# Performance work log

Measured on AMD Instinct MI355X. Metric: run time of the kernel, lower is better.

The kernel has to match this reference:

```python
import jax, jax.numpy as jnp
import numpy as np

B, NNODE, FIN, FOUT = 64, 512, 64, 64

def setup_inputs() -> dict:
    key = jax.random.key(0)
    ks = jax.random.split(key, 8)
    stdW = 1.0 / np.sqrt(FIN)
    stdA = 1.0 / np.sqrt(FOUT)
    return {
        "X": jax.random.normal(ks[0], (B, NNODE, FIN), dtype=jnp.float32),
        "A": jax.random.uniform(ks[1], (B, NNODE, NNODE), dtype=jnp.float32),
        "N": jax.random.randint(ks[2], (B,), 1, NNODE + 1, dtype=jnp.int64),
        "W": jax.random.uniform(ks[3], (FIN, FOUT), jnp.float32, -stdW, stdW),
        "a": jax.random.uniform(ks[4], (FOUT, FOUT), jnp.float32, -stdA, stdA),
        "bias_W": jax.random.uniform(ks[5], (FOUT,), jnp.float32, -stdW, stdW),
        "bias_a": jax.random.uniform(ks[6], (NNODE,), jnp.float32, -1.0 / np.sqrt(NNODE), 1.0 / np.sqrt(NNODE)),
    }

def reference(X, A, N, W, a, bias_W, bias_a):
    # A_ = A + identity on the top-left n_atoms block (only diagonal entries)
    idx = jnp.arange(A.shape[1])
    diag_mask = (idx[None, :] < N[:, None]).astype(A.dtype)  # [B, n]
    A_ = A + jnp.einsum('bn,nm->bnm', diag_mask, jnp.eye(A.shape[1], dtype=A.dtype))
    # XW: [B, n, F_out]
    XW = jnp.einsum('bnc,cd->bnd', X, W)
    # buf[a,j,k] = sum_i a[i,j] * XW^T[a,j,k]  (einsum 'ij,ajk->ajk')
    col_sum = a.sum(axis=0)  # [F_out]
    XWT = jnp.swapaxes(XW, 1, 2)  # [B, F_out, n]
    buf = col_sum[None, :, None] * XWT
    Z = jnp.einsum('bif,bfk->bik', XW, buf) + bias_a  # [B, n, n] + [n] broadcast on last dim
    att = jnp.tanh(jnp.einsum('bij,bjk->bik', A_, Z))
    H = jnp.einsum('bij,bjd->bid', att, XW) + bias_W
    return H
```

## Files before the change

kernel.cpp:

```cpp
#include <hip/hip_runtime.h>

#define BB 64
#define NN 512
#define FD 64

typedef short bf16x8 __attribute__((ext_vector_type(8)));
typedef float f32x4 __attribute__((ext_vector_type(4)));

__device__ __forceinline__ unsigned short f2bf(float f){
    unsigned u = __builtin_bit_cast(unsigned, f);
    u += 0x7fffu + ((u >> 16) & 1u);
    return (unsigned short)(u >> 16);
}
__device__ __forceinline__ float bf2f(unsigned short h){
    unsigned u = ((unsigned)h) << 16;
    return __builtin_bit_cast(float, u);
}
__device__ __forceinline__ float fast_tanh(float x){
    float e = __expf(2.0f * x);
    return 1.0f - 2.0f * __builtin_amdgcn_rcpf(e + 1.0f);
}

__global__ __launch_bounds__(256) void k_xw(const float* __restrict__ X,
                                            const float* __restrict__ W,
                                            unsigned short* __restrict__ XWh,
                                            unsigned short* __restrict__ XWt){
    __shared__ unsigned short Xl[64][72];
    __shared__ unsigned short Wtl[64][72];
    __shared__ unsigned short Cl[64][72];
    __shared__ unsigned short ClT[64][72];
    int t = threadIdx.x;
    int row0 = blockIdx.x * 64;
    int r = t >> 2, c0 = (t & 3) * 16;
    {
        const float4* wsrc = (const float4*)&W[r*64 + c0];
        #pragma unroll
        for (int q = 0; q < 4; q++){
            float4 v = wsrc[q];
            Wtl[c0 + q*4 + 0][r] = f2bf(v.x);
            Wtl[c0 + q*4 + 1][r] = f2bf(v.y);
            Wtl[c0 + q*4 + 2][r] = f2bf(v.z);
            Wtl[c0 + q*4 + 3][r] = f2bf(v.w);
        }
        const float4* src = (const float4*)&X[(row0 + r)*FD + c0];
        #pragma unroll
        for (int q = 0; q < 4; q++){
            float4 v = src[q];
            ushort4 h; h.x=f2bf(v.x); h.y=f2bf(v.y); h.z=f2bf(v.z); h.w=f2bf(v.w);
            *(ushort4*)&Xl[r][c0 + q*4] = h;
        }
    }
    __syncthreads();
    int lane = t & 63, w = t >> 6, l15 = lane & 15, quad = lane >> 4;
    f32x4 acc[4] = {{0,0,0,0},{0,0,0,0},{0,0,0,0},{0,0,0,0}};
    #pragma unroll
    for (int ks = 0; ks < 2; ks++){
        bf16x8 af = *(const bf16x8*)&Xl[w*16 + l15][ks*32 + quad*8];
        #pragma unroll
        for (int nt = 0; nt < 4; nt++){
            bf16x8 bfr = *(const bf16x8*)&Wtl[nt*16 + l15][ks*32 + quad*8];
            acc[nt] = __builtin_amdgcn_mfma_f32_16x16x32_bf16(af, bfr, acc[nt], 0, 0, 0);
        }
    }
    #pragma unroll
    for (int nt = 0; nt < 4; nt++)
        #pragma unroll
        for (int rg = 0; rg < 4; rg++){
            unsigned short hb = f2bf(acc[nt][rg]);
            Cl [w*16 + quad*4 + rg][nt*16 + l15] = hb;
            ClT[nt*16 + l15][w*16 + quad*4 + rg] = hb;
        }
    __syncthreads();
    int b = blockIdx.x >> 3, n0 = (blockIdx.x & 7) * 64;
    {
        uint4 v0 = *(const uint4*)&Cl[r][c0];
        uint4 v1 = *(const uint4*)&Cl[r][c0 + 8];
        *(uint4*)&XWh[(row0 + r)*FD + c0]     = v0;
        *(uint4*)&XWh[(row0 + r)*FD + c0 + 8] = v1;
    }
    {
        uint4 v0 = *(const uint4*)&ClT[r][c0];
        uint4 v1 = *(const uint4*)&ClT[r][c0 + 8];
        *(uint4*)&XWt[(b*64 + r)*NN + n0 + c0]     = v0;
        *(uint4*)&XWt[(b*64 + r)*NN + n0 + c0 + 8] = v1;
    }
}

__global__ __launch_bounds__(512, 6) void k_fused(const float* __restrict__ A,
                                                  const unsigned short* __restrict__ XWh,
                                                  const unsigned short* __restrict__ XWt,
                                                  const float* __restrict__ a,
                                                  const int* __restrict__ Ni,
                                                  const float* __restrict__ bias_a,
                                                  const float* __restrict__ bias_W,
                                                  float* __restrict__ H){
    __shared__ unsigned short buf[4][64][72];
    __shared__ float cspart[8][64];
    __shared__ float csl[64];
    __shared__ float rspart[64][8];
    __shared__ float rsl[64];
    __shared__ float bl[512];
    int t = threadIdx.x;
    int b = blockIdx.x, it = blockIdx.y;
    int i0 = it * 64;
    int Nb = (Ni[1] == 0) ? Ni[2*b] : Ni[b];
    int lane = t & 63, w = t >> 6, l15 = lane & 15, quad = lane >> 4;
    int wr = w & 3, wc = w >> 2;
    int r8 = t >> 3, c4 = (t & 7) * 4, c8 = (t & 7) * 8;
    const float* Ab = A + (b*NN + i0)*NN;
    const unsigned short* XWtb = XWt + b*64*NN;
    const unsigned short* XWhb = XWh + b*NN*FD;

    {
        int cd = t & 63, cp = t >> 6;
        float s = 0.f;
        #pragma unroll
        for (int i = 0; i < 8; i++) s += a[(cp*8 + i)*64 + cd];
        cspart[cp][cd] = s;
    }
    bl[t] = bias_a[t];

    float4 pA[2][2]; uint4 pB;
    pA[0][0] = *(const float4*)&Ab[r8*NN + c4];
    pA[0][1] = *(const float4*)&Ab[r8*NN + 32 + c4];
    pA[1][0] = *(const float4*)&Ab[r8*NN + 64 + c4];
    pA[1][1] = *(const float4*)&Ab[r8*NN + 64 + 32 + c4];
    pB = *(const uint4*)&XWtb[r8*NN + c8];
    f32x4 acc[2] = {{0,0,0,0},{0,0,0,0}};
    float rs = 0.f;
    #pragma unroll
    for (int c = 0; c < 8; c++){
        {
            float4 v = pA[c & 1][0];
            rs += v.x + v.y + v.z + v.w;
            ushort4 h; h.x=f2bf(v.x); h.y=f2bf(v.y); h.z=f2bf(v.z); h.w=f2bf(v.w);
            *(ushort4*)&buf[c & 1][r8][c4] = h;
            v = pA[c & 1][1];
            rs += v.x + v.y + v.z + v.w;
            ushort4 h2; h2.x=f2bf(v.x); h2.y=f2bf(v.y); h2.z=f2bf(v.z); h2.w=f2bf(v.w);
            *(ushort4*)&buf[c & 1][r8][32 + c4] = h2;
        }
        *(uint4*)&buf[2 + (c & 1)][r8][c8] = pB;
        if (c < 7) pB = *(const uint4*)&XWtb[r8*NN + (c+1)*64 + c8];
        __syncthreads();
        if (c < 6){
            pA[c & 1][0] = *(const float4*)&Ab[r8*NN + (c+2)*64 + c4];
            pA[c & 1][1] = *(const float4*)&Ab[r8*NN + (c+2)*64 + 32 + c4];
        }
        #pragma unroll
        for (int ks = 0; ks < 2; ks++){
            bf16x8 af = *(const bf16x8*)&buf[c & 1][wr*16 + l15][ks*32 + quad*8];
            #pragma unroll
            for (int nt = 0; nt < 2; nt++){
                bf16x8 bfr = *(const bf16x8*)&buf[2 + (c & 1)][wc*32 + nt*16 + l15][ks*32 + quad*8];
                acc[nt] = __builtin_amdgcn_mfma_f32_16x16x32_bf16(af, bfr, acc[nt], 0, 0, 0);
            }
        }
        if (c == it){
            #pragma unroll
            for (int nt = 0; nt < 2; nt++)
                #pragma unroll
                for (int rg = 0; rg < 4; rg++){
                    int iloc = wr*16 + quad*4 + rg;
                    if (i0 + iloc < Nb)
                        acc[nt][rg] += bf2f(buf[2 + (c & 1)][wc*32 + nt*16 + l15][iloc]);
                }
        }
    }
    rspart[r8][t & 7] = rs;
    __syncthreads();
    if (t < 64){
        float s = 0.f;
        #pragma unroll
        for (int p = 0; p < 8; p++) s += cspart[p][t];
        csl[t] = s;
    } else if (t < 128){
        int row = t - 64;
        float s = 0.f;
        #pragma unroll
        for (int p = 0; p < 8; p++) s += rspart[row][p];
        if (i0 + row < Nb) s += 1.f;
        rsl[row] = s;
    }
    __syncthreads();
    #pragma unroll
    for (int nt = 0; nt < 2; nt++){
        float cs = csl[wc*32 + nt*16 + l15];
        #pragma unroll
        for (int rg = 0; rg < 4; rg++)
            buf[2][wr*16 + quad*4 + rg][wc*32 + nt*16 + l15] = f2bf(acc[nt][rg] * cs);
    }
    __syncthreads();
    bf16x8 maf[2];
    maf[0] = *(const bf16x8*)&buf[2][wr*16 + l15][quad*8];
    maf[1] = *(const bf16x8*)&buf[2][wr*16 + l15][32 + quad*8];
    float rs_r[4];
    #pragma unroll
    for (int rg = 0; rg < 4; rg++) rs_r[rg] = rsl[wr*16 + quad*4 + rg];

    {
        uint4 q1 = *(const uint4*)&XWhb[r8*FD + c8];
        uint4 q2 = *(const uint4*)&XWtb[r8*NN + c8];
        *(uint4*)&buf[0][r8][c8] = q1;
        *(uint4*)&buf[1][r8][c8] = q2;
    }
    uint4 q1 = *(const uint4*)&XWhb[(64 + r8)*FD + c8];
    uint4 q2 = *(const uint4*)&XWtb[r8*NN + 64 + c8];
    f32x4 hacc[2] = {{0,0,0,0},{0,0,0,0}};
    #pragma unroll
    for (int jt = 0; jt < 8; jt++){
        __syncthreads();
        #pragma unroll
        for (int nt = 0; nt < 2; nt++){
            float bv = bl[jt*64 + wc*32 + nt*16 + l15];
            f32x4 arg = { rs_r[0]*bv, rs_r[1]*bv, rs_r[2]*bv, rs_r[3]*bv };
            #pragma unroll
            for (int ks = 0; ks < 2; ks++){
                bf16x8 bfr = *(const bf16x8*)&buf[0][wc*32 + nt*16 + l15][ks*32 + quad*8];
                arg = __builtin_amdgcn_mfma_f32_16x16x32_bf16(maf[ks], bfr, arg, 0, 0, 0);
            }
            #pragma unroll
            for (int rg = 0; rg < 4; rg++)
                buf[2][wr*16 + quad*4 + rg][wc*32 + nt*16 + l15] = f2bf(fast_tanh(arg[rg]));
        }
        __syncthreads();
        {
            const unsigned short (*bT)[72] = buf[(jt & 1) ? 3 : 1];
            #pragma unroll
            for (int ks = 0; ks < 2; ks++){
                bf16x8 paf = *(const bf16x8*)&buf[2][wr*16 + l15][ks*32 + quad*8];
                #pragma unroll
                for (int dt = 0; dt < 2; dt++){
                    bf16x8 bfr = *(const bf16x8*)&bT[wc*32 + dt*16 + l15][ks*32 + quad*8];
                    hacc[dt] = __builtin_amdgcn_mfma_f32_16x16x32_bf16(paf, bfr, hacc[dt], 0, 0, 0);
                }
            }
        }
        if (jt < 7){
            *(uint4*)&buf[0][r8][c8] = q1;
            *(uint4*)&buf[(jt & 1) ? 1 : 3][r8][c8] = q2;
            if (jt < 6){
                q1 = *(const uint4*)&XWhb[((jt+2)*64 + r8)*FD + c8];
                q2 = *(const uint4*)&XWtb[r8*NN + (jt+2)*64 + c8];
            }
        }
    }
    #pragma unroll
    for (int dt = 0; dt < 2; dt++){
        float bw = bias_W[wc*32 + dt*16 + l15];
        #pragma unroll
        for (int rg = 0; rg < 4; rg++)
            H[(b*NN + i0 + wr*16 + quad*4 + rg)*FD + wc*32 + dt*16 + l15] = hacc[dt][rg] + bw;
    }
}

extern "C" void kernel_launch(void* const* d_in, const int* in_sizes, int n_in,
                              void* d_out, int out_size, void* d_ws, size_t ws_size,
                              hipStream_t stream){
    const float* X      = (const float*)d_in[0];
    const float* A      = (const float*)d_in[1];
    const int*   N      = (const int*)  d_in[2];
    const float* W      = (const float*)d_in[3];
    const float* a      = (const float*)d_in[4];
    const float* bias_W = (const float*)d_in[5];
    const float* bias_a = (const float*)d_in[6];
    float* H = (float*)d_out;
    char* ws = (char*)d_ws;

    unsigned short* XWh = (unsigned short*)(ws);
    unsigned short* XWt = (unsigned short*)(ws + (4u<<20));

    k_xw   <<<BB * NN / 64, 256, 0, stream>>>(X, W, XWh, XWt);
    k_fused<<<dim3(BB, 8), 512, 0, stream>>>(A, XWh, XWt, a, N, bias_a, bias_W, H);
}
```

Baseline: 138.5 us.

## Load MFMA B operands directly from global into registers, drop LDS staging

B-operand fragments (XW^T and XW) are now loaded straight from global memory into per-lane MFMA registers with one-tile-ahead prefetch, instead of being staged through shared memory. This halves the LDS buffer and removes one barrier per iteration in the second loop by double-buffering the tanh tile. A custom barrier waits only on LDS counters so in-flight global loads are not drained. The trade-off is redundant global and L2 traffic, since each wave reloads its own fragments, plus higher register pressure under the 6-blocks launch bound.

```diff
diff --git a/kernel.cpp b/kernel.cpp
--- a/kernel.cpp
+++ b/kernel.cpp
@@ -19,6 +19,12 @@
 __device__ __forceinline__ float fast_tanh(float x){
     float e = __expf(2.0f * x);
     return 1.0f - 2.0f * __builtin_amdgcn_rcpf(e + 1.0f);
+}
+__device__ __forceinline__ void bar_lds(){
+    asm volatile("" ::: "memory");
+    __builtin_amdgcn_s_waitcnt(0xC07F);
+    __builtin_amdgcn_s_barrier();
+    asm volatile("" ::: "memory");
 }
 
 __global__ __launch_bounds__(256) void k_xw(const float* __restrict__ X,
@@ -94,7 +100,7 @@
                                                   const float* __restrict__ bias_a,
                                                   const float* __restrict__ bias_W,
                                                   float* __restrict__ H){
-    __shared__ unsigned short buf[4][64][72];
+    __shared__ unsigned short buf[2][64][72];
     __shared__ float cspart[8][64];
     __shared__ float csl[64];
     __shared__ float rspart[64][8];
@@ -106,7 +112,7 @@
     int Nb = (Ni[1] == 0) ? Ni[2*b] : Ni[b];
     int lane = t & 63, w = t >> 6, l15 = lane & 15, quad = lane >> 4;
     int wr = w & 3, wc = w >> 2;
-    int r8 = t >> 3, c4 = (t & 7) * 4, c8 = (t & 7) * 8;
+    int r8 = t >> 3, c4 = (t & 7) * 4;
     const float* Ab = A + (b*NN + i0)*NN;
     const unsigned short* XWtb = XWt + b*64*NN;
     const unsigned short* XWhb = XWh + b*NN*FD;
@@ -120,12 +126,17 @@
     }
     bl[t] = bias_a[t];
 
-    float4 pA[2][2]; uint4 pB;
+    float4 pA[2][2];
     pA[0][0] = *(const float4*)&Ab[r8*NN + c4];
     pA[0][1] = *(const float4*)&Ab[r8*NN + 32 + c4];
     pA[1][0] = *(const float4*)&Ab[r8*NN + 64 + c4];
     pA[1][1] = *(const float4*)&Ab[r8*NN + 64 + 32 + c4];
-    pB = *(const uint4*)&XWtb[r8*NN + c8];
+    bf16x8 nB[2][2];
+    #pragma unroll
+    for (int ks = 0; ks < 2; ks++)
+        #pragma unroll
+        for (int nt = 0; nt < 2; nt++)
+            nB[ks][nt] = *(const bf16x8*)&XWtb[(wc*32 + nt*16 + l15)*NN + ks*32 + quad*8];
     f32x4 acc[2] = {{0,0,0,0},{0,0,0,0}};
     float rs = 0.f;
     #pragma unroll
@@ -140,35 +151,42 @@
             ushort4 h2; h2.x=f2bf(v.x); h2.y=f2bf(v.y); h2.z=f2bf(v.z); h2.w=f2bf(v.w);
             *(ushort4*)&buf[c & 1][r8][32 + c4] = h2;
         }
-        *(uint4*)&buf[2 + (c & 1)][r8][c8] = pB;
-        if (c < 7) pB = *(const uint4*)&XWtb[r8*NN + (c+1)*64 + c8];
-        __syncthreads();
+        bar_lds();
         if (c < 6){
             pA[c & 1][0] = *(const float4*)&Ab[r8*NN + (c+2)*64 + c4];
             pA[c & 1][1] = *(const float4*)&Ab[r8*NN + (c+2)*64 + 32 + c4];
         }
+        bf16x8 uB[2][2];
+        #pragma unroll
+        for (int ks = 0; ks < 2; ks++)
+            #pragma unroll
+            for (int nt = 0; nt < 2; nt++)
+                uB[ks][nt] = nB[ks][nt];
+        if (c < 7){
+            #pragma unroll
+            for (int ks = 0; ks < 2; ks++)
+                #pragma unroll
+                for (int nt = 0; nt < 2; nt++)
+                    nB[ks][nt] = *(const bf16x8*)&XWtb[(wc*32 + nt*16 + l15)*NN + (c+1)*64 + ks*32 + quad*8];
+        }
         #pragma unroll
         for (int ks = 0; ks < 2; ks++){
             bf16x8 af = *(const bf16x8*)&buf[c & 1][wr*16 + l15][ks*32 + quad*8];
             #pragma unroll
-            for (int nt = 0; nt < 2; nt++){
-                bf16x8 bfr = *(const bf16x8*)&buf[2 + (c & 1)][wc*32 + nt*16 + l15][ks*32 + quad*8];
-                acc[nt] = __builtin_amdgcn_mfma_f32_16x16x32_bf16(af, bfr, acc[nt], 0, 0, 0);
-            }
-        }
-        if (c == it){
-            #pragma unroll
             for (int nt = 0; nt < 2; nt++)
-                #pragma unroll
-                for (int rg = 0; rg < 4; rg++){
-                    int iloc = wr*16 + quad*4 + rg;
-                    if (i0 + iloc < Nb)
-                        acc[nt][rg] += bf2f(buf[2 + (c & 1)][wc*32 + nt*16 + l15][iloc]);
-                }
-        }
-    }
+                acc[nt] = __builtin_amdgcn_mfma_f32_16x16x32_bf16(af, uB[ks][nt], acc[nt], 0, 0, 0);
+        }
+    }
+    #pragma unroll
+    for (int nt = 0; nt < 2; nt++)
+        #pragma unroll
+        for (int rg = 0; rg < 4; rg++){
+            int iloc = wr*16 + quad*4 + rg;
+            if (i0 + iloc < Nb)
+                acc[nt][rg] += bf2f(XWtb[(wc*32 + nt*16 + l15)*NN + i0 + iloc]);
+        }
     rspart[r8][t & 7] = rs;
-    __syncthreads();
+    bar_lds();
     if (t < 64){
         float s = 0.f;
         #pragma unroll
@@ -182,67 +200,72 @@
         if (i0 + row < Nb) s += 1.f;
         rsl[row] = s;
     }
-    __syncthreads();
+    bar_lds();
     #pragma unroll
     for (int nt = 0; nt < 2; nt++){
         float cs = csl[wc*32 + nt*16 + l15];
         #pragma unroll
         for (int rg = 0; rg < 4; rg++)
-            buf[2][wr*16 + quad*4 + rg][wc*32 + nt*16 + l15] = f2bf(acc[nt][rg] * cs);
-    }
-    __syncthreads();
+            buf[0][wr*16 + quad*4 + rg][wc*32 + nt*16 + l15] = f2bf(acc[nt][rg] * cs);
+    }
+    bar_lds();
     bf16x8 maf[2];
-    maf[0] = *(const bf16x8*)&buf[2][wr*16 + l15][quad*8];
-    maf[1] = *(const bf16x8*)&buf[2][wr*16 + l15][32 + quad*8];
+    maf[0] = *(const bf16x8*)&buf[0][wr*16 + l15][quad*8];
+    maf[1] = *(const bf16x8*)&buf[0][wr*16 + l15][32 + quad*8];
     float rs_r[4];
     #pragma unroll
     for (int rg = 0; rg < 4; rg++) rs_r[rg] = rsl[wr*16 + quad*4 + rg];
 
-    {
-        uint4 q1 = *(const uint4*)&XWhb[r8*FD + c8];
-        uint4 q2 = *(const uint4*)&XWtb[r8*NN + c8];
-        *(uint4*)&buf[0][r8][c8] = q1;
-        *(uint4*)&buf[1][r8][c8] = q2;
-    }
-    uint4 q1 = *(const uint4*)&XWhb[(64 + r8)*FD + c8];
-    uint4 q2 = *(const uint4*)&XWtb[r8*NN + 64 + c8];
+    bf16x8 g1[2][2], g2[2][2];
+    #pragma unroll
+    for (int ks = 0; ks < 2; ks++)
+        #pragma unroll
+        for (int nt = 0; nt < 2; nt++){
+            g1[ks][nt] = *(const bf16x8*)&XWhb[(wc*32 + nt*16 + l15)*FD + ks*32 + quad*8];
+            g2[ks][nt] = *(const bf16x8*)&XWtb[(wc*32 + nt*16 + l15)*NN + ks*32 + quad*8];
+        }
     f32x4 hacc[2] = {{0,0,0,0},{0,0,0,0}};
     #pragma unroll
     for (int jt = 0; jt < 8; jt++){
-        __syncthreads();
+        int ps = (jt & 1) ^ 1;
+        f32x4 arg[2];
         #pragma unroll
         for (int nt = 0; nt < 2; nt++){
             float bv = bl[jt*64 + wc*32 + nt*16 + l15];
-            f32x4 arg = { rs_r[0]*bv, rs_r[1]*bv, rs_r[2]*bv, rs_r[3]*bv };
-            #pragma unroll
-            for (int ks = 0; ks < 2; ks++){
-                bf16x8 bfr = *(const bf16x8*)&buf[0][wc*32 + nt*16 + l15][ks*32 + quad*8];
-                arg = __builtin_amdgcn_mfma_f32_16x16x32_bf16(maf[ks], bfr, arg, 0, 0, 0);
-            }
+            arg[nt][0] = rs_r[0]*bv; arg[nt][1] = rs_r[1]*bv;
+            arg[nt][2] = rs_r[2]*bv; arg[nt][3] = rs_r[3]*bv;
+        }
+        #pragma unroll
+        for (int ks = 0; ks < 2; ks++)
+            #pragma unroll
+            for (int nt = 0; nt < 2; nt++)
+                arg[nt] = __builtin_amdgcn_mfma_f32_16x16x32_bf16(maf[ks], g1[ks][nt], arg[nt], 0, 0, 0);
+        if (jt < 7){
+            #pragma unroll
+            for (int ks = 0; ks < 2; ks++)
+                #pragma unroll
+                for (int nt = 0; nt < 2; nt++)
+                    g1[ks][nt] = *(const bf16x8*)&XWhb[((jt+1)*64 + wc*32 + nt*16 + l15)*FD + ks*32 + quad*8];
+        }
+        #pragma unroll
+        for (int nt = 0; nt < 2; nt++)
             #pragma unroll
             for (int rg = 0; rg < 4; rg++)
-                buf[2][wr*16 + quad*4 + rg][wc*32 + nt*16 + l15] = f2bf(fast_tanh(arg[rg]));
-        }
-        __syncthreads();
-        {
-            const unsigned short (*bT)[72] = buf[(jt & 1) ? 3 : 1];
-            #pragma unroll
-            for (int ks = 0; ks < 2; ks++){
-                bf16x8 paf = *(const bf16x8*)&buf[2][wr*16 + l15][ks*32 + quad*8];
+                buf[ps][wr*16 + quad*4 + rg][wc*32 + nt*16 + l15] = f2bf(fast_tanh(arg[nt][rg]));
+        bar_lds();
+        #pragma unroll
+        for (int ks = 0; ks < 2; ks++){
+            bf16x8 paf = *(const bf16x8*)&buf[ps][wr*16 + l15][ks*32 + quad*8];
+            #pragma unroll
+            for (int dt = 0; dt < 2; dt++)
+                hacc[dt] = __builtin_amdgcn_mfma_f32_16x16x32_bf16(paf, g2[ks][dt], hacc[dt], 0, 0, 0);
+        }
+        if (jt < 7){
+            #pragma unroll
+            for (int ks = 0; ks < 2; ks++)
                 #pragma unroll
-                for (int dt = 0; dt < 2; dt++){
-                    bf16x8 bfr = *(const bf16x8*)&bT[wc*32 + dt*16 + l15][ks*32 + quad*8];
-                    hacc[dt] = __builtin_amdgcn_mfma_f32_16x16x32_bf16(paf, bfr, hacc[dt], 0, 0, 0);
-                }
-            }
-        }
-        if (jt < 7){
-            *(uint4*)&buf[0][r8][c8] = q1;
-            *(uint4*)&buf[(jt & 1) ? 1 : 3][r8][c8] = q2;
-            if (jt < 6){
-                q1 = *(const uint4*)&XWhb[((jt+2)*64 + r8)*FD + c8];
-                q2 = *(const uint4*)&XWtb[r8*NN + (jt+2)*64 + c8];
-            }
+                for (int dt = 0; dt < 2; dt++)
+                    g2[ks][dt] = *(const bf16x8*)&XWtb[(wc*32 + dt*16 + l15)*NN + (jt+1)*64 + ks*32 + quad*8];
         }
     }
     #pragma unroll
```

New measurement: 163.2 us. 1.18x slower.
